# Kernel tuning notes

Measured on AMD Instinct MI355X. Metric: run time of the kernel, lower is better.

## Reference

```python
import jax, jax.numpy as jnp
import numpy as np

DIM = 512
D_IN = 4096
N_OBJ = 2048
N_REL = 32768
STEPS = 2
N_OBJ_CLS = 151
N_REL_CLS = 51
EPS = 1e-5


def _mlp2(x, w1, b1, w2, b2):
    # Linear -> ReLU -> Linear (torch Linear: y = x W^T + b)
    return jnp.maximum(x @ w1.T + b1, 0.0) @ w2.T + b2


def _gate(a, b, w, bias):
    # Sequential(Linear(2*dim, 1), Sigmoid) on cat([a, b], 1)
    return jax.nn.sigmoid(jnp.concatenate([a, b], axis=1) @ w.T + bias)


def _gru_cell(x, h, wih, whh, bih, bhh):
    gi = x @ wih.T + bih  # [N, 3*DIM]
    gh = h @ whh.T + bhh
    ir, iz, inew = jnp.split(gi, 3, axis=1)
    hr, hz, hnew = jnp.split(gh, 3, axis=1)
    r = jax.nn.sigmoid(ir + hr)
    z = jax.nn.sigmoid(iz + hz)
    n = jnp.tanh(inew + r * hnew)
    return (1.0 - z) * n + z * h


def setup_inputs() -> dict:
    key = jax.random.key(0)
    ks = jax.random.split(key, 32)
    rn = lambda k, shape, s=0.02: jax.random.normal(k, shape, dtype=jnp.float32) * s
    z = lambda *shape: jnp.zeros(shape, dtype=jnp.float32)
    return {
        'x_obj': jax.random.normal(ks[0], (N_OBJ, D_IN), dtype=jnp.float32),
        'x_pred': jax.random.normal(ks[1], (N_REL, D_IN), dtype=jnp.float32),
        'rel_inds': jax.random.randint(ks[2], (N_REL, 2), 0, N_OBJ),
        # obj / pred embedding MLPs
        'oe_w1': rn(ks[3], (DIM, D_IN)), 'oe_b1': z(DIM),
        'oe_w2': rn(ks[4], (DIM, DIM)), 'oe_b2': z(DIM),
        'pe_w1': rn(ks[5], (DIM, D_IN)), 'pe_b1': z(DIM),
        'pe_w2': rn(ks[6], (DIM, DIM)), 'pe_b2': z(DIM),
        # gates: Linear(2*dim, 1)
        'g_sn_w': rn(ks[7], (1, 2 * DIM)), 'g_sn_b': z(1),
        'g_on_w': rn(ks[8], (1, 2 * DIM)), 'g_on_b': z(1),
        'g_se_w': rn(ks[9], (1, 2 * DIM)), 'g_se_b': z(1),
        'g_oe_w': rn(ks[10], (1, 2 * DIM)), 'g_oe_b': z(1),
        # GRU cells
        'ngru_wih': rn(ks[11], (3 * DIM, DIM)), 'ngru_whh': rn(ks[12], (3 * DIM, DIM)),
        'ngru_bih': z(3 * DIM), 'ngru_bhh': z(3 * DIM),
        'egru_wih': rn(ks[13], (3 * DIM, DIM)), 'egru_whh': rn(ks[14], (3 * DIM, DIM)),
        'egru_bih': z(3 * DIM), 'egru_bhh': z(3 * DIM),
        # classifier heads
        'op_w': rn(ks[15], (N_OBJ_CLS, DIM)), 'op_b': z(N_OBJ_CLS),
        'pp_w': rn(ks[16], (N_REL_CLS, DIM)), 'pp_b': z(N_REL_CLS),
    }


def reference(x_obj, x_pred, rel_inds,
              oe_w1, oe_b1, oe_w2, oe_b2,
              pe_w1, pe_b1, pe_w2, pe_b2,
              g_sn_w, g_sn_b, g_on_w, g_on_b,
              g_se_w, g_se_b, g_oe_w, g_oe_b,
              ngru_wih, ngru_whh, ngru_bih, ngru_bhh,
              egru_wih, egru_whh, egru_bih, egru_bhh,
              op_w, op_b, pp_w, pp_b):
    n_obj = x_obj.shape[0]
    subj_idx = rel_inds[:, 0]
    obj_idx = rel_inds[:, 1]

    h_obj = _mlp2(x_obj, oe_w1, oe_b1, oe_w2, oe_b2)    # [N_obj, DIM]
    h_edge = _mlp2(x_pred, pe_w1, pe_b1, pe_w2, pe_b2)  # [N_rel, DIM]

    # row sums of the 0/1 subj/obj_pred_map == in-degree counts (constants)
    ones = jnp.ones((rel_inds.shape[0],), dtype=jnp.float32)
    cnt_s = jax.ops.segment_sum(ones, subj_idx, num_segments=n_obj)[:, None]
    cnt_o = jax.ops.segment_sum(ones, obj_idx, num_segments=n_obj)[:, None]

    for _ in range(STEPS):
        sub_vert = h_obj[subj_idx]  # [N_rel, DIM]
        obj_vert = h_obj[obj_idx]

        # node update: gated edge->node messages, mean-aggregated per node
        msg_p2s = _gate(sub_vert, h_edge, g_sn_w, g_sn_b) * h_edge
        msg_p2o = _gate(obj_vert, h_edge, g_on_w, g_on_b) * h_edge
        node_message = (
            jax.ops.segment_sum(msg_p2s, subj_idx, num_segments=n_obj) / (cnt_s + EPS)
            + jax.ops.segment_sum(msg_p2o, obj_idx, num_segments=n_obj) / (cnt_o + EPS)
        ) / 2.0
        new_h_obj = _gru_cell(node_message, h_obj, ngru_wih, ngru_whh, ngru_bih, ngru_bhh)

        # edge update: gated node->edge messages
        msg_s2p = _gate(sub_vert, h_edge, g_se_w, g_se_b) * sub_vert
        msg_o2p = _gate(obj_vert, h_edge, g_oe_w, g_oe_b) * obj_vert
        edge_message = (msg_s2p + msg_o2p) / 2.0
        h_edge = _gru_cell(edge_message, h_edge, egru_wih, egru_whh, egru_bih, egru_bhh)
        h_obj = new_h_obj

    obj_class_logits = h_obj @ op_w.T + op_b    # [N_obj, 151]
    pred_class_logits = h_edge @ pp_w.T + pp_b  # [N_rel, 51]
    obj_class_labels = jnp.argmax(obj_class_logits[:, 1:], axis=1) + 1
    return (h_obj, h_edge, obj_class_logits, pred_class_logits, obj_class_labels, rel_inds)
```

## Files before the change

### kernel.cpp

```cpp
#include <hip/hip_runtime.h>
#include <math.h>

typedef unsigned short u16;
typedef unsigned int u32;
typedef _Float16 f16;
typedef f16 f16x8 __attribute__((ext_vector_type(8)));
typedef float f32x4 __attribute__((ext_vector_type(4)));

#define DIM 512
#define D_IN 4096
#define N_OBJS 2048
#define N_RELS 32768
#define N_OBJ_CLS 151
#define N_REL_CLS 51
#define EPSV 1e-5f

#define OFF_HOBJ  0
#define OFF_HEDGE (N_OBJS*DIM)
#define OFF_OLOG  (OFF_HEDGE + N_RELS*DIM)
#define OFF_PLOG  (OFF_OLOG + N_OBJS*N_OBJ_CLS)
#define OFF_LBL   (OFF_PLOG + N_RELS*N_REL_CLS)
#define OFF_RI    (OFF_LBL + N_OBJS)

__device__ __forceinline__ float sigmoidf_(float x) { return 1.0f / (1.0f + expf(-x)); }
__device__ __forceinline__ u16 f2h_(float f) {
    union { f16 h; u16 u; } c; c.h = (f16)f; return c.u;
}
__device__ __forceinline__ float h2f_(u16 u) {
    union { f16 h; u16 u; } c; c.u = u; return (float)c.h;
}

__device__ __forceinline__ void cvt8h1(const float* f, uint4& h) {
    u32 hh[8];
#pragma unroll
    for (int i = 0; i < 8; i++) hh[i] = f2h_(f[i]);
    h.x = hh[0] | (hh[1] << 16); h.y = hh[2] | (hh[3] << 16);
    h.z = hh[4] | (hh[5] << 16); h.w = hh[6] | (hh[7] << 16);
}
__device__ __forceinline__ void cvt8h2(const float* f, uint4& h, uint4& l) {
    u32 hh[8], ll[8];
#pragma unroll
    for (int i = 0; i < 8; i++) {
        u16 x = f2h_(f[i]);
        hh[i] = x;
        ll[i] = f2h_(f[i] - h2f_(x));
    }
    h.x = hh[0] | (hh[1] << 16); h.y = hh[2] | (hh[3] << 16);
    h.z = hh[4] | (hh[5] << 16); h.w = hh[6] | (hh[7] << 16);
    l.x = ll[0] | (ll[1] << 16); l.y = ll[2] | (ll[3] << 16);
    l.z = ll[4] | (ll[5] << 16); l.w = ll[6] | (ll[7] << 16);
}

__device__ __forceinline__ int swzo(int row, int c) {
    return row * 32 + ((c ^ ((row >> 1) & 3)) << 3);
}

__device__ __forceinline__ int xcdswz(int orig, int nwg) {
    const int q = nwg >> 3;
    return (orig & 7) * q + (orig >> 3);
}

__device__ __forceinline__ void gload16(const void* g, void* l) {
    __builtin_amdgcn_global_load_lds(
        (const __attribute__((address_space(1))) void*)g,
        (__attribute__((address_space(3))) void*)l, 16, 0, 0);
}

__global__ __launch_bounds__(256) void convert_h(const float* __restrict__ src,
    u16* __restrict__ hi, int n4)
{
    const int i = blockIdx.x * 256 + threadIdx.x;
    if (i >= n4) return;
    const float4 v = ((const float4*)src)[i];
    ((ushort4*)hi)[i] = make_ushort4(f2h_(v.x), f2h_(v.y), f2h_(v.z), f2h_(v.w));
}

template<bool RELU, int AT, bool WSPLIT>
__device__ __forceinline__ void gemm_a32_body(
    int id, u16* sAh, u16* sBh, u16* sAl,
    const float* __restrict__ A, const u16* __restrict__ Bhi,
    const float* __restrict__ bias, u16* __restrict__ Chi, u16* __restrict__ Clo,
    int NX, int K)
{
    const int m0 = (id / NX) * 128, n0 = (id % NX) * 128;
    const int N = NX * 128;
    const int t = threadIdx.x;
    const int wid = t >> 6, lane = t & 63;
    const int wm = (wid >> 1) * 64, wn = (wid & 1) * 64;
    const int lr = lane & 15, lk = lane >> 4;

    f32x4 acc[4][4] = {};

    const int sr = t >> 1;
    const int sc = (t & 1) * 2;
    const float* Ap = A + (size_t)(m0 + sr) * K + (t & 1) * 16;

    const int rB = (wid * 2) * 16 + (lane >> 2);
    const int cB = (lane & 3) ^ ((rB >> 1) & 3);
    const u16* Bp0 = Bhi + (size_t)(n0 + rB) * K + cB * 8;
    const u16* Bp1 = Bp0 + (size_t)16 * K;
    u16* Bd0 = &sBh[(wid * 2) * 512];
    u16* Bd1 = Bd0 + 512;

    float fv[16];
    *(float4*)&fv[0]  = *(const float4*)(Ap);
    *(float4*)&fv[4]  = *(const float4*)(Ap + 4);
    *(float4*)&fv[8]  = *(const float4*)(Ap + 8);
    *(float4*)&fv[12] = *(const float4*)(Ap + 12);

    for (int k0 = 0; k0 < K; k0 += 32) {
        uint4 ah0, ah1, al0, al1;
        if (AT == 2) { cvt8h2(fv, ah0, al0); cvt8h2(fv + 8, ah1, al1); }
        else         { cvt8h1(fv, ah0);      cvt8h1(fv + 8, ah1); }

        __syncthreads();
        gload16(Bp0 + k0, Bd0);
        gload16(Bp1 + k0, Bd1);
        *(uint4*)&sAh[swzo(sr, sc)]     = ah0;
        *(uint4*)&sAh[swzo(sr, sc + 1)] = ah1;
        if (AT == 2) {
            *(uint4*)&sAl[swzo(sr, sc)]     = al0;
            *(uint4*)&sAl[swzo(sr, sc + 1)] = al1;
        }
        asm volatile("s_waitcnt vmcnt(0)" ::: "memory");
        __syncthreads();

        const int kn = k0 + 32;
        if (kn < K) {
            *(float4*)&fv[0]  = *(const float4*)(Ap + kn);
            *(float4*)&fv[4]  = *(const float4*)(Ap + kn + 4);
            *(float4*)&fv[8]  = *(const float4*)(Ap + kn + 8);
            *(float4*)&fv[12] = *(const float4*)(Ap + kn + 12);
        }

        f16x8 ah[4], al[4], bh[4];
#pragma unroll
        for (int f = 0; f < 4; f++) {
            const int off = swzo(wm + f * 16 + lr, lk);
            ah[f] = *(const f16x8*)&sAh[off];
            if (AT == 2) al[f] = *(const f16x8*)&sAl[off];
            bh[f] = *(const f16x8*)&sBh[swzo(wn + f * 16 + lr, lk)];
        }
#pragma unroll
        for (int fm = 0; fm < 4; fm++)
#pragma unroll
            for (int fn = 0; fn < 4; fn++) {
                acc[fm][fn] = __builtin_amdgcn_mfma_f32_16x16x32_f16(ah[fm], bh[fn], acc[fm][fn], 0, 0, 0);
                if (AT == 2)
                    acc[fm][fn] = __builtin_amdgcn_mfma_f32_16x16x32_f16(al[fm], bh[fn], acc[fm][fn], 0, 0, 0);
            }
    }
#pragma unroll
    for (int fm = 0; fm < 4; fm++) {
        const int mrow = m0 + wm + fm * 16 + lk * 4;
#pragma unroll
        for (int fn = 0; fn < 4; fn++) {
            const int col = n0 + wn + fn * 16 + lr;
            const float bv = bias[col];
#pragma unroll
            for (int j = 0; j < 4; j++) {
                float v = acc[fm][fn][j] + bv;
                if (RELU) v = fmaxf(v, 0.0f);
                const u16 h = f2h_(v);
                Chi[(size_t)(mrow + j) * N + col] = h;
                if (WSPLIT) Clo[(size_t)(mrow + j) * N + col] = f2h_(v - h2f_(h));
            }
        }
    }
}

__global__ __launch_bounds__(256, 3) void enc1_both(
    const float* __restrict__ xp, const u16* __restrict__ pw,
    const float* __restrict__ pb, u16* __restrict__ tmpe,
    const float* __restrict__ xo, const u16* __restrict__ ow,
    const float* __restrict__ ob, u16* __restrict__ tmpoh, u16* __restrict__ tmpol)
{
    __shared__ u16 smem[3 * 4096];
    const int id = xcdswz(blockIdx.x, gridDim.x);
    if (id < 1024)
        gemm_a32_body<true, 1, false>(id, smem, smem + 4096, nullptr,
                                      xp, pw, pb, tmpe, nullptr, 4, D_IN);
    else
        gemm_a32_body<true, 2, true>(id - 1024, smem, smem + 4096, smem + 8192,
                                     xo, ow, ob, tmpoh, tmpol, 4, D_IN);
}

template<int AT, bool WF32, bool WHI, bool WLO>
__device__ __forceinline__ void gemm_f16_body(
    int id, u16* smem,
    const u16* __restrict__ Ahi, const u16* __restrict__ Alo,
    const u16* __restrict__ Bhi, const float* __restrict__ bias,
    float* __restrict__ C32, u16* __restrict__ Chi, u16* __restrict__ Clo,
    int NX, int N, int ldc, int K)
{
    const int m0 = (id / NX) * 128, n0 = (id % NX) * 128;
    const int t = threadIdx.x;
    const int wid = t >> 6, lane = t & 63;
    const int wm = (wid >> 1) * 64, wn = (wid & 1) * 64;
    const int lr = lane & 15, lk = lane >> 4;

    f32x4 acc[4][4] = {};

    const int rr = (wid * 2) * 16 + (lane >> 2);
    const int cc = (lane & 3) ^ ((rr >> 1) & 3);
    const u16* pA0 = Ahi + (size_t)(m0 + rr) * K + cc * 8;
    const u16* pA1 = pA0 + (size_t)16 * K;
    const u16* pL0 = (AT == 2) ? Alo + (size_t)(m0 + rr) * K + cc * 8 : nullptr;
    const u16* pL1 = (AT == 2) ? pL0 + (size_t)16 * K : nullptr;
    const u16* pB0 = Bhi + (size_t)(n0 + rr) * K + cc * 8;
    const u16* pB1 = pB0 + (size_t)16 * K;
    const int bOff = (wid * 2) * 512;

    for (int k0 = 0; k0 < K; k0 += 64) {
        __syncthreads();
#pragma unroll
        for (int h = 0; h < 2; h++) {
            const int kk = k0 + h * 32;
            u16* sA_ = smem + h * 4096;
            u16* sB_ = smem + 8192 + h * 4096;
            gload16(pA0 + kk, sA_ + bOff);
            gload16(pA1 + kk, sA_ + bOff + 512);
            if (AT == 2) {
                u16* sL_ = smem + 16384 + h * 4096;
                gload16(pL0 + kk, sL_ + bOff);
                gload16(pL1 + kk, sL_ + bOff + 512);
            }
            gload16(pB0 + kk, sB_ + bOff);
            gload16(pB1 + kk, sB_ + bOff + 512);
        }
        asm volatile("s_waitcnt vmcnt(0)" ::: "memory");
        __syncthreads();

#pragma unroll
        for (int h = 0; h < 2; h++) {
            const u16* sA_ = smem + h * 4096;
            const u16* sB_ = smem + 8192 + h * 4096;
            const u16* sL_ = smem + 16384 + h * 4096;
            f16x8 ah[4], al[4], bh[4];
#pragma unroll
            for (int f = 0; f < 4; f++) {
                const int off = swzo(wm + f * 16 + lr, lk);
                ah[f] = *(const f16x8*)&sA_[off];
                if (AT == 2) al[f] = *(const f16x8*)&sL_[off];
                bh[f] = *(const f16x8*)&sB_[swzo(wn + f * 16 + lr, lk)];
            }
#pragma unroll
            for (int fm = 0; fm < 4; fm++)
#pragma unroll
                for (int fn = 0; fn < 4; fn++) {
                    acc[fm][fn] = __builtin_amdgcn_mfma_f32_16x16x32_f16(ah[fm], bh[fn], acc[fm][fn], 0, 0, 0);
                    if (AT == 2)
                        acc[fm][fn] = __builtin_amdgcn_mfma_f32_16x16x32_f16(al[fm], bh[fn], acc[fm][fn], 0, 0, 0);
                }
        }
    }
#pragma unroll
    for (int fm = 0; fm < 4; fm++) {
        const int mrow = m0 + wm + fm * 16 + lk * 4;
#pragma unroll
        for (int fn = 0; fn < 4; fn++) {
            const int col = n0 + wn + fn * 16 + lr;
            const float bv = bias[col];
#pragma unroll
            for (int j = 0; j < 4; j++) {
                const float v = acc[fm][fn][j] + bv;
                if (WF32 && col < N) C32[(size_t)(mrow + j) * ldc + col] = v;
                if (WHI) {
                    const u16 h = f2h_(v);
                    Chi[(size_t)(mrow + j) * (NX * 128) + col] = h;
                    if (WLO)
                        Clo[(size_t)(mrow + j) * (NX * 128) + col] = f2h_(v - h2f_(h));
                }
            }
        }
    }
}

template<int AT, bool WF32, bool WHI, bool WLO>
__global__ __launch_bounds__(256, AT == 1 ? 4 : 3) void gemm_f16(
    const u16* __restrict__ Ahi, const u16* __restrict__ Alo,
    const u16* __restrict__ Bhi, const float* __restrict__ bias,
    float* __restrict__ C32, u16* __restrict__ Chi, u16* __restrict__ Clo,
    int NX, int N, int ldc, int K)
{
    __shared__ u16 smem[AT == 2 ? 6 * 4096 : 4 * 4096];
    const int id = xcdswz(blockIdx.x, gridDim.x);
    gemm_f16_body<AT, WF32, WHI, WLO>(id, smem, Ahi, Alo, Bhi, bias,
                                      C32, Chi, Clo, NX, N, ldc, K);
}

__global__ __launch_bounds__(256, 3) void cls_both(
    const u16* __restrict__ hhe, const u16* __restrict__ pph,
    const float* __restrict__ ppb, float* __restrict__ plog,
    const u16* __restrict__ hhoh, const u16* __restrict__ hhol,
    const u16* __restrict__ oph, const float* __restrict__ opb,
    float* __restrict__ olog)
{
    __shared__ u16 smem[6 * 4096];
    const int id = xcdswz(blockIdx.x, gridDim.x);
    if (id < 256)
        gemm_f16_body<1, true, false, false>(id, smem, hhe, nullptr, pph, ppb,
                                             plog, nullptr, nullptr,
                                             1, N_REL_CLS, N_REL_CLS, DIM);
    else
        gemm_f16_body<2, true, false, false>(id - 256, smem, hhoh, hhol, oph, opb,
                                             olog, nullptr, nullptr,
                                             2, N_OBJ_CLS, N_OBJ_CLS, DIM);
}

template<int AT>
__global__ __launch_bounds__(256, AT == 1 ? 4 : 3) void gru_gemm2(
    const u16* __restrict__ Xh, const u16* __restrict__ Xl,
    const u16* __restrict__ WiH, const float* __restrict__ bi, u16* __restrict__ gi,
    const u16* __restrict__ Hh, const u16* __restrict__ Hl,
    const u16* __restrict__ WhH, const float* __restrict__ bhs, u16* __restrict__ gh_,
    int K)
{
    __shared__ u16 smem[AT == 2 ? 6 * 4096 : 4 * 4096];
    const int id = xcdswz(blockIdx.x, gridDim.x);
    const int part = id % 24;
    const int m0b = id / 24;
    const bool isH = part >= 12;
    const u16* Ahi = isH ? Hh : Xh;
    const u16* Alo = isH ? Hl : Xl;
    const u16* Bhi = isH ? WhH : WiH;
    const float* bias = isH ? bhs : bi;
    u16* C = isH ? gh_ : gi;
    const int nblk = part - (isH ? 12 : 0);
    gemm_f16_body<AT, false, true, false>(m0b * 12 + nblk, smem,
                                          Ahi, Alo, Bhi, bias,
                                          nullptr, C, nullptr, 12, 1536, 1536, K);
}

__device__ __forceinline__ float gcomb(u16 ir, u16 iz, u16 in_, u16 hr, u16 hz,
                                       u16 hn, float h) {
    const float r = sigmoidf_(h2f_(ir) + h2f_(hr));
    const float z = sigmoidf_(h2f_(iz) + h2f_(hz));
    const float n = tanhf(h2f_(in_) + r * h2f_(hn));
    return (1.0f - z) * n + z * h;
}

template<bool WSPLIT, bool WF32>
__global__ __launch_bounds__(256) void gru_combine(
    const u16* __restrict__ gi, const u16* __restrict__ gh,
    u16* __restrict__ hh, u16* __restrict__ hl, float* __restrict__ H32, int R)
{
    const int idx = blockIdx.x * 256 + threadIdx.x;
    if (idx >= R * 128) return;
    const int r = idx >> 7, c4 = (idx & 127) * 4;
    const size_t gb = (size_t)r * 1536 + c4;
    const ushort4 ir4 = *(const ushort4*)&gi[gb];
    const ushort4 iz4 = *(const ushort4*)&gi[gb + 512];
    const ushort4 in4 = *(const ushort4*)&gi[gb + 1024];
    const ushort4 hr4 = *(const ushort4*)&gh[gb];
    const ushort4 hz4 = *(const ushort4*)&gh[gb + 512];
    const ushort4 hn4 = *(const ushort4*)&gh[gb + 1024];
    const size_t hb = (size_t)r * 512 + c4;
    const ushort4 hhi = *(const ushort4*)&hh[hb];
    float h0 = h2f_(hhi.x), h1 = h2f_(hhi.y), h2 = h2f_(hhi.z), h3 = h2f_(hhi.w);
    if (WSPLIT) {
        const ushort4 hlo = *(const ushort4*)&hl[hb];
        h0 += h2f_(hlo.x); h1 += h2f_(hlo.y); h2 += h2f_(hlo.z); h3 += h2f_(hlo.w);
    }
    float4 o;
    o.x = gcomb(ir4.x, iz4.x, in4.x, hr4.x, hz4.x, hn4.x, h0);
    o.y = gcomb(ir4.y, iz4.y, in4.y, hr4.y, hz4.y, hn4.y, h1);
    o.z = gcomb(ir4.z, iz4.z, in4.z, hr4.z, hz4.z, hn4.z, h2);
    o.w = gcomb(ir4.w, iz4.w, in4.w, hr4.w, hz4.w, hn4.w, h3);
    const ushort4 hi4 = make_ushort4(f2h_(o.x), f2h_(o.y), f2h_(o.z), f2h_(o.w));
    *(ushort4*)&hh[hb] = hi4;
    if (WSPLIT) {
        *(ushort4*)&hl[hb] = make_ushort4(
            f2h_(o.x - h2f_(hi4.x)), f2h_(o.y - h2f_(hi4.y)),
            f2h_(o.z - h2f_(hi4.z)), f2h_(o.w - h2f_(hi4.w)));
    }
    if (WF32) *(float4*)&H32[hb] = o;
}

__global__ __launch_bounds__(256) void count_int(const int* __restrict__ rel,
                                                 int* cs, int* co)
{
    const int e = blockIdx.x * 256 + threadIdx.x;
    atomicAdd(&cs[rel[2 * e]], 1);
    atomicAdd(&co[rel[2 * e + 1]], 1);
}

__global__ __launch_bounds__(256) void scan_off(const int* __restrict__ cs,
    const int* __restrict__ co, int* __restrict__ offs, int* __restrict__ offo)
{
    __shared__ int tmp[256];
    for (int arr = 0; arr < 2; arr++) {
        const int* c = arr ? co : cs;
        int* off = arr ? offo : offs;
        const int base = threadIdx.x * 8;
        int loc[8]; int s = 0;
#pragma unroll
        for (int j = 0; j < 8; j++) { loc[j] = c[base + j]; s += loc[j]; }
        tmp[threadIdx.x] = s;
        __syncthreads();
        for (int d = 1; d < 256; d <<= 1) {
            const int v = (threadIdx.x >= d) ? tmp[threadIdx.x - d] : 0;
            __syncthreads();
            tmp[threadIdx.x] += v;
            __syncthreads();
        }
        int p = tmp[threadIdx.x] - s;
#pragma unroll
        for (int j = 0; j < 8; j++) { off[base + j] = p; p += loc[j]; }
        __syncthreads();
    }
}

__global__ __launch_bounds__(256) void fill_csr(const int* __restrict__ rel,
    int* curS, int* curO, const int* __restrict__ offs, const int* __restrict__ offo,
    int* __restrict__ listS, int* __restrict__ listO)
{
    const int e = blockIdx.x * 256 + threadIdx.x;
    const int s = rel[2 * e], o = rel[2 * e + 1];
    const int i = atomicAdd(&curS[s], 1);
    listS[offs[s] + i] = e;
    const int j = atomicAdd(&curO[o], 1);
    listO[offo[o] + j] = e;
}

__global__ __launch_bounds__(256) void gatepass(
    const u16* __restrict__ hho, const u16* __restrict__ hhe,
    const int* __restrict__ rel,
    const float* __restrict__ wsn, const float* __restrict__ bsn,
    const float* __restrict__ won, const float* __restrict__ bon,
    const float* __restrict__ wse, const float* __restrict__ bse,
    const float* __restrict__ woe, const float* __restrict__ boe,
    const int* __restrict__ cs, const int* __restrict__ co,
    u16* __restrict__ emh, float* __restrict__ af, float* __restrict__ ag)
{
    const int e = blockIdx.x * 4 + (threadIdx.x >> 6);
    const int lane = threadIdx.x & 63;
    const int s = rel[2 * e], o = rel[2 * e + 1];
    const int c = lane * 8;

    const uint4 hsu = *(const uint4*)&hho[(size_t)s * DIM + c];
    const uint4 hou = *(const uint4*)&hho[(size_t)o * DIM + c];
    const uint4 heu = *(const uint4*)&hhe[(size_t)e * DIM + c];
    float hs[8], ho[8], he[8];
    hs[0] = h2f_((u16)hsu.x); hs[1] = h2f_((u16)(hsu.x >> 16));
    hs[2] = h2f_((u16)hsu.y); hs[3] = h2f_((u16)(hsu.y >> 16));
    hs[4] = h2f_((u16)hsu.z); hs[5] = h2f_((u16)(hsu.z >> 16));
    hs[6] = h2f_((u16)hsu.w); hs[7] = h2f_((u16)(hsu.w >> 16));
    ho[0] = h2f_((u16)hou.x); ho[1] = h2f_((u16)(hou.x >> 16));
    ho[2] = h2f_((u16)hou.y); ho[3] = h2f_((u16)(hou.y >> 16));
    ho[4] = h2f_((u16)hou.z); ho[5] = h2f_((u16)(hou.z >> 16));
    ho[6] = h2f_((u16)hou.w); ho[7] = h2f_((u16)(hou.w >> 16));
    he[0] = h2f_((u16)heu.x); he[1] = h2f_((u16)(heu.x >> 16));
    he[2] = h2f_((u16)heu.y); he[3] = h2f_((u16)(heu.y >> 16));
    he[4] = h2f_((u16)heu.z); he[5] = h2f_((u16)(heu.z >> 16));
    he[6] = h2f_((u16)heu.w); he[7] = h2f_((u16)(heu.w >> 16));

    float p0 = 0.f, p1 = 0.f, p2 = 0.f, p3 = 0.f;
#pragma unroll
    for (int q = 0; q < 2; q++) {
        const float4 w0v = *(const float4*)&wsn[c + q * 4];
        const float4 w0e = *(const float4*)&wsn[DIM + c + q * 4];
        const float4 w1v = *(const float4*)&won[c + q * 4];
        const float4 w1e = *(const float4*)&won[DIM + c + q * 4];
        const float4 w2v = *(const float4*)&wse[c + q * 4];
        const float4 w2e = *(const float4*)&wse[DIM + c + q * 4];
        const float4 w3v = *(const float4*)&woe[c + q * 4];
        const float4 w3e = *(const float4*)&woe[DIM + c + q * 4];
        const float* s4 = &hs[q * 4];
        const float* o4 = &ho[q * 4];
        const float* e4 = &he[q * 4];
        p0 += s4[0]*w0v.x + s4[1]*w0v.y + s4[2]*w0v.z + s4[3]*w0v.w
            + e4[0]*w0e.x + e4[1]*w0e.y + e4[2]*w0e.z + e4[3]*w0e.w;
        p1 += o4[0]*w1v.x + o4[1]*w1v.y + o4[2]*w1v.z + o4[3]*w1v.w
            + e4[0]*w1e.x + e4[1]*w1e.y + e4[2]*w1e.z + e4[3]*w1e.w;
        p2 += s4[0]*w2v.x + s4[1]*w2v.y + s4[2]*w2v.z + s4[3]*w2v.w
            + e4[0]*w2e.x + e4[1]*w2e.y + e4[2]*w2e.z + e4[3]*w2e.w;
        p3 += o4[0]*w3v.x + o4[1]*w3v.y + o4[2]*w3v.z + o4[3]*w3v.w
            + e4[0]*w3e.x + e4[1]*w3e.y + e4[2]*w3e.z + e4[3]*w3e.w;
    }
#pragma unroll
    for (int off = 32; off; off >>= 1) {
        p0 += __shfl_xor(p0, off);
        p1 += __shfl_xor(p1, off);
        p2 += __shfl_xor(p2, off);
        p3 += __shfl_xor(p3, off);
    }
    const float gsn = sigmoidf_(p0 + bsn[0]);
    const float gon = sigmoidf_(p1 + bon[0]);
    const float gse = sigmoidf_(p2 + bse[0]);
    const float goe = sigmoidf_(p3 + boe[0]);

    if (lane == 0) {
        af[e] = 0.5f * gsn / ((float)cs[s] + EPSV);
        ag[e] = 0.5f * gon / ((float)co[o] + EPSV);
    }
    u16 em8[8];
#pragma unroll
    for (int j = 0; j < 8; j++)
        em8[j] = f2h_(0.5f * (gse * hs[j] + goe * ho[j]));
    *(uint4*)&emh[(size_t)e * DIM + c] = *(const uint4*)em8;
}

__global__ __launch_bounds__(256) void gather_nm(
    const u16* __restrict__ hhe,
    const int* __restrict__ listS, const int* __restrict__ listO,
    const int* __restrict__ offs, const int* __restrict__ offo,
    const int* __restrict__ cs, const int* __restrict__ co,
    const float* __restrict__ af, const float* __restrict__ ag,
    u16* __restrict__ nmh, u16* __restrict__ nml)
{
    const int v = blockIdx.x * 4 + (threadIdx.x >> 6);
    const int lane = threadIdx.x & 63;
    const int c = lane * 8;

    float acc[8] = {};
#pragma unroll
    for (int side = 0; side < 2; side++) {
        const int* list = side ? listO : listS;
        const int b = side ? offo[v] : offs[v];
        const int n = side ? co[v] : cs[v];
        const float* coef = side ? ag : af;
        for (int i = 0; i < n; i++) {
            const int e = list[b + i];
            const float a = coef[e];
            const uint4 x = *(const uint4*)&hhe[(size_t)e * DIM + c];
            acc[0] += a * h2f_((u16)x.x); acc[1] += a * h2f_((u16)(x.x >> 16));
            acc[2] += a * h2f_((u16)x.y); acc[3] += a * h2f_((u16)(x.y >> 16));
            acc[4] += a * h2f_((u16)x.z); acc[5] += a * h2f_((u16)(x.z >> 16));
            acc[6] += a * h2f_((u16)x.w); acc[7] += a * h2f_((u16)(x.w >> 16));
        }
    }
    u16 hi8[8], lo8[8];
#pragma unroll
    for (int j = 0; j < 8; j++) {
        hi8[j] = f2h_(acc[j]);
        lo8[j] = f2h_(acc[j] - h2f_(hi8[j]));
    }
    *(uint4*)&nmh[(size_t)v * DIM + c] = *(const uint4*)hi8;
    *(uint4*)&nml[(size_t)v * DIM + c] = *(const uint4*)lo8;
}

__global__ __launch_bounds__(256) void argmax_kernel(const float* __restrict__ logits,
                                                     float* __restrict__ out)
{
    const int row = blockIdx.x * 4 + (threadIdx.x >> 6);
    const int lane = threadIdx.x & 63;
    float bv = -1e30f; int bi = 1;
    for (int j = 1 + lane; j < N_OBJ_CLS; j += 64) {
        const float v = logits[(size_t)row * N_OBJ_CLS + j];
        if (v > bv) { bv = v; bi = j; }
    }
#pragma unroll
    for (int off = 32; off; off >>= 1) {
        const float ov = __shfl_xor(bv, off);
        const int oi = __shfl_xor(bi, off);
        if (ov > bv || (ov == bv && oi < bi)) { bv = ov; bi = oi; }
    }
    if (lane == 0) out[row] = (float)bi;
}

__global__ __launch_bounds__(256) void relinds_kernel(const int* __restrict__ rel,
                                                      float* __restrict__ out)
{
    const int i = blockIdx.x * 256 + threadIdx.x;
    out[i] = (float)rel[i];
}

extern "C" void kernel_launch(void* const* d_in, const int* in_sizes, int n_in,
                              void* d_out, int out_size, void* d_ws, size_t ws_size,
                              hipStream_t stream)
{
    const float* x_obj = (const float*)d_in[0];
    const float* x_pred = (const float*)d_in[1];
    const int* rel = (const int*)d_in[2];
    const float* oe_w1 = (const float*)d_in[3];
    const float* oe_b1 = (const float*)d_in[4];
    const float* oe_w2 = (const float*)d_in[5];
    const float* oe_b2 = (const float*)d_in[6];
    const float* pe_w1 = (const float*)d_in[7];
    const float* pe_b1 = (const float*)d_in[8];
    const float* pe_w2 = (const float*)d_in[9];
    const float* pe_b2 = (const float*)d_in[10];
    const float* g_sn_w = (const float*)d_in[11];
    const float* g_sn_b = (const float*)d_in[12];
    const float* g_on_w = (const float*)d_in[13];
    const float* g_on_b = (const float*)d_in[14];
    const float* g_se_w = (const float*)d_in[15];
    const float* g_se_b = (const float*)d_in[16];
    const float* g_oe_w = (const float*)d_in[17];
    const float* g_oe_b = (const float*)d_in[18];
    const float* ngru_wih = (const float*)d_in[19];
    const float* ngru_whh = (const float*)d_in[20];
    const float* ngru_bih = (const float*)d_in[21];
    const float* ngru_bhh = (const float*)d_in[22];
    const float* egru_wih = (const float*)d_in[23];
    const float* egru_whh = (const float*)d_in[24];
    const float* egru_bih = (const float*)d_in[25];
    const float* egru_bhh = (const float*)d_in[26];
    const float* op_w = (const float*)d_in[27];
    const float* op_b = (const float*)d_in[28];
    const float* pp_w = (const float*)d_in[29];
    const float* pp_b = (const float*)d_in[30];

    float* out = (float*)d_out;

    float* h_obj = out + OFF_HOBJ;
    float* h_edge = out + OFF_HEDGE;

    char* wsp = (char*)d_ws;
    float* af = (float*)wsp; wsp += N_RELS * 4;
    float* ag = (float*)wsp; wsp += N_RELS * 4;
    int* cs = (int*)wsp;   wsp += N_OBJS * 4;
    int* co = (int*)wsp;   wsp += N_OBJS * 4;
    int* offs = (int*)wsp; wsp += N_OBJS * 4;
    int* offo = (int*)wsp; wsp += N_OBJS * 4;
    int* curS = (int*)wsp; wsp += N_OBJS * 4;
    int* curO = (int*)wsp; wsp += N_OBJS * 4;
    int* listS = (int*)wsp; wsp += N_RELS * 4;
    int* listO = (int*)wsp; wsp += N_RELS * 4;

    u16* wp = (u16*)wsp;
    const int s_big = DIM * D_IN, s_sq = DIM * DIM, s_gru = 3 * DIM * DIM;
    u16 *oe1h = wp; wp += s_big;
    u16 *pe1h = wp; wp += s_big;
    u16 *oe2h = wp; wp += s_sq;
    u16 *pe2h = wp; wp += s_sq;
    u16 *nih_h = wp; wp += s_gru;
    u16 *nhh_h = wp; wp += s_gru;
    u16 *eih_h = wp; wp += s_gru;
    u16 *ehh_h = wp; wp += s_gru;
    u16 *oph = wp; wp += 256 * DIM;
    u16 *pph = wp; wp += 128 * DIM;
    u16 *tmpo_h = wp; wp += (size_t)N_OBJS * DIM;
    u16 *tmpo_l = wp; wp += (size_t)N_OBJS * DIM;
    u16 *tmpe_h = wp; wp += (size_t)N_RELS * DIM;
    u16 *hhoh = wp; wp += (size_t)N_OBJS * DIM;
    u16 *hhol = wp; wp += (size_t)N_OBJS * DIM;
    u16 *hhe  = wp; wp += (size_t)N_RELS * DIM;
    u16 *emh  = wp; wp += (size_t)N_RELS * DIM;
    u16 *nmh  = wp; wp += (size_t)N_OBJS * DIM;
    u16 *nml  = wp; wp += (size_t)N_OBJS * DIM;

    const size_t used = (size_t)((char*)wp - (char*)d_ws);
    int R = 8192;
    if (used + (size_t)16384 * 6144 <= ws_size) R = 16384;
    u16* gi = wp;
    u16* gh = gi + (size_t)R * 1536;

    auto cvtw = [&](const float* s, u16* h, int n) {
        convert_h<<<(n / 4 + 255) / 256, 256, 0, stream>>>(s, h, n / 4);
    };
    cvtw(oe_w1, oe1h, s_big);
    cvtw(pe_w1, pe1h, s_big);
    cvtw(oe_w2, oe2h, s_sq);
    cvtw(pe_w2, pe2h, s_sq);
    cvtw(ngru_wih, nih_h, s_gru);
    cvtw(ngru_whh, nhh_h, s_gru);
    cvtw(egru_wih, eih_h, s_gru);
    cvtw(egru_whh, ehh_h, s_gru);
    cvtw(op_w, oph, N_OBJ_CLS * DIM);
    cvtw(pp_w, pph, N_REL_CLS * DIM);

    hipMemsetAsync(cs, 0, 2 * N_OBJS * sizeof(int), stream);
    hipMemsetAsync(curS, 0, 2 * N_OBJS * sizeof(int), stream);
    count_int<<<N_RELS / 256, 256, 0, stream>>>(rel, cs, co);
    scan_off<<<1, 256, 0, stream>>>(cs, co, offs, offo);
    fill_csr<<<N_RELS / 256, 256, 0, stream>>>(rel, curS, curO, offs, offo, listS, listO);

    enc1_both<<<1088, 256, 0, stream>>>(
        x_pred, pe1h, pe_b1, tmpe_h,
        x_obj, oe1h, oe_b1, tmpo_h, tmpo_l);
    gemm_f16<1, false, true, false><<<4 * (N_RELS / 128), 256, 0, stream>>>(
        tmpe_h, nullptr, pe2h, pe_b2, nullptr, hhe, nullptr, 4, DIM, DIM, DIM);
    gemm_f16<2, false, true, true><<<4 * (N_OBJS / 128), 256, 0, stream>>>(
        tmpo_h, tmpo_l, oe2h, oe_b2, nullptr, hhoh, hhol, 4, DIM, DIM, DIM);

    for (int step = 0; step < 2; step++) {
        gatepass<<<N_RELS / 4, 256, 0, stream>>>(
            hhoh, hhe, rel,
            g_sn_w, g_sn_b, g_on_w, g_on_b, g_se_w, g_se_b, g_oe_w, g_oe_b,
            cs, co, emh, af, ag);
        gather_nm<<<N_OBJS / 4, 256, 0, stream>>>(
            hhe, listS, listO, offs, offo, cs, co, af, ag, nmh, nml);

        gru_gemm2<2><<<24 * (N_OBJS / 128), 256, 0, stream>>>(
            nmh, nml, nih_h, ngru_bih, gi, hhoh, hhol, nhh_h, ngru_bhh, gh, DIM);
        if (step == 0)
            gru_combine<true, false><<<(N_OBJS * 128 + 255) / 256, 256, 0, stream>>>(
                gi, gh, hhoh, hhol, nullptr, N_OBJS);
        else
            gru_combine<true, true><<<(N_OBJS * 128 + 255) / 256, 256, 0, stream>>>(
                gi, gh, hhoh, hhol, h_obj, N_OBJS);

        for (int r0 = 0; r0 < N_RELS; r0 += R) {
            const int Rc = (N_RELS - r0 < R) ? (N_RELS - r0) : R;
            gru_gemm2<1><<<24 * (Rc / 128), 256, 0, stream>>>(
                emh + (size_t)r0 * DIM, nullptr, eih_h, egru_bih, gi,
                hhe + (size_t)r0 * DIM, nullptr, ehh_h, egru_bhh, gh, DIM);
            if (step == 0)
                gru_combine<false, false><<<(Rc * 128 + 255) / 256, 256, 0, stream>>>(
                    gi, gh, hhe + (size_t)r0 * DIM, nullptr, nullptr, Rc);
            else
                gru_combine<false, true><<<(Rc * 128 + 255) / 256, 256, 0, stream>>>(
                    gi, gh, hhe + (size_t)r0 * DIM, nullptr, h_edge + (size_t)r0 * DIM, Rc);
        }
    }

    cls_both<<<288, 256, 0, stream>>>(
        hhe, pph, pp_b, out + OFF_PLOG,
        hhoh, hhol, oph, op_b, out + OFF_OLOG);

    argmax_kernel<<<N_OBJS / 4, 256, 0, stream>>>(out + OFF_OLOG, out + OFF_LBL);
    relinds_kernel<<<(2 * N_RELS) / 256, 256, 0, stream>>>(rel, out + OFF_RI);
}
```

Baseline: 1.002 ms.

## Fuse GRU r/z gate GEMMs over concatenated [x,h] with packed weights

Concatenates the input and hidden rows along K and packs the r/z slices of W_ih and W_hh into one 1024x1024 weight, so the r and z pre-activations come out of a single K=1024 GEMM with summed biases. The n-gate input and hidden parts stay as separate K=512 GEMMs. All outputs go to one 2048-wide buffer, and the combine kernel reads four slices instead of six. This cuts GEMM output writes and combine reads from 3072 to 2048 columns per row with the same FLOPs, at the cost of a new GEMM body and extra weight packing kernels.

```diff
diff --git a/kernel.cpp b/kernel.cpp
--- a/kernel.cpp
+++ b/kernel.cpp
@@ -14,6 +14,7 @@
 #define N_OBJ_CLS 151
 #define N_REL_CLS 51
 #define EPSV 1e-5f
+#define GOUT 2048
 
 #define OFF_HOBJ  0
 #define OFF_HEDGE (N_OBJS*DIM)
@@ -73,6 +74,23 @@
     if (i >= n4) return;
     const float4 v = ((const float4*)src)[i];
     ((ushort4*)hi)[i] = make_ushort4(f2h_(v.x), f2h_(v.y), f2h_(v.z), f2h_(v.w));
+}
+
+__global__ __launch_bounds__(256) void pack_rz(const u16* __restrict__ ih,
+    const u16* __restrict__ hh, u16* __restrict__ wrz)
+{
+    const int idx = blockIdx.x * 256 + threadIdx.x;
+    const int n = idx >> 7, kk = (idx & 127) * 8;
+    const uint4 v = (kk < 512) ? *(const uint4*)&ih[(size_t)n * 512 + kk]
+                               : *(const uint4*)&hh[(size_t)n * 512 + kk - 512];
+    *(uint4*)&wrz[(size_t)n * 1024 + kk] = v;
+}
+
+__global__ __launch_bounds__(256) void pack_brz(const float* __restrict__ bih,
+    const float* __restrict__ bhh, float* __restrict__ brz)
+{
+    const int j = blockIdx.x * 256 + threadIdx.x;
+    brz[j] = bih[j] + bhh[j];
 }
 
 template<bool RELU, int AT, bool WSPLIT>
@@ -309,52 +327,134 @@
 }
 
 template<int AT>
-__global__ __launch_bounds__(256, AT == 1 ? 4 : 3) void gru_gemm2(
+__device__ __forceinline__ void gru_body(
+    int m0b, int nblk, u16* smem,
     const u16* __restrict__ Xh, const u16* __restrict__ Xl,
-    const u16* __restrict__ WiH, const float* __restrict__ bi, u16* __restrict__ gi,
     const u16* __restrict__ Hh, const u16* __restrict__ Hl,
-    const u16* __restrict__ WhH, const float* __restrict__ bhs, u16* __restrict__ gh_,
-    int K)
+    const u16* __restrict__ B, const float* __restrict__ bias,
+    u16* __restrict__ C, int K)
+{
+    const int m0 = m0b * 128, n0 = nblk * 128;
+    const int t = threadIdx.x;
+    const int wid = t >> 6, lane = t & 63;
+    const int wm = (wid >> 1) * 64, wn = (wid & 1) * 64;
+    const int lr = lane & 15, lk = lane >> 4;
+
+    f32x4 acc[4][4] = {};
+
+    const int rr = (wid * 2) * 16 + (lane >> 2);
+    const int cc = (lane & 3) ^ ((rr >> 1) & 3);
+    const size_t arow = (size_t)(m0 + rr) * DIM + cc * 8;
+    const u16* pX0 = Xh + arow; const u16* pX1 = pX0 + 16 * DIM;
+    const u16* pXl0 = (AT == 2) ? Xl + arow : nullptr;
+    const u16* pXl1 = (AT == 2) ? pXl0 + 16 * DIM : nullptr;
+    const u16* pH0 = Hh + arow; const u16* pH1 = pH0 + 16 * DIM;
+    const u16* pHl0 = (AT == 2) ? Hl + arow : nullptr;
+    const u16* pHl1 = (AT == 2) ? pHl0 + 16 * DIM : nullptr;
+    const u16* pB0 = B + (size_t)(n0 + rr) * K + cc * 8;
+    const u16* pB1 = pB0 + (size_t)16 * K;
+    const int bOff = (wid * 2) * 512;
+
+    for (int k0 = 0; k0 < K; k0 += 64) {
+        __syncthreads();
+#pragma unroll
+        for (int h = 0; h < 2; h++) {
+            const int kk = k0 + h * 32;
+            const bool inX = kk < 512;
+            const int ka = inX ? kk : kk - 512;
+            u16* sA_ = smem + h * 4096;
+            u16* sB_ = smem + 8192 + h * 4096;
+            gload16((inX ? pX0 : pH0) + ka, sA_ + bOff);
+            gload16((inX ? pX1 : pH1) + ka, sA_ + bOff + 512);
+            if (AT == 2) {
+                u16* sL_ = smem + 16384 + h * 4096;
+                gload16((inX ? pXl0 : pHl0) + ka, sL_ + bOff);
+                gload16((inX ? pXl1 : pHl1) + ka, sL_ + bOff + 512);
+            }
+            gload16(pB0 + kk, sB_ + bOff);
+            gload16(pB1 + kk, sB_ + bOff + 512);
+        }
+        asm volatile("s_waitcnt vmcnt(0)" ::: "memory");
+        __syncthreads();
+
+#pragma unroll
+        for (int h = 0; h < 2; h++) {
+            const u16* sA_ = smem + h * 4096;
+            const u16* sB_ = smem + 8192 + h * 4096;
+            const u16* sL_ = smem + 16384 + h * 4096;
+            f16x8 ah[4], al[4], bh[4];
+#pragma unroll
+            for (int f = 0; f < 4; f++) {
+                const int off = swzo(wm + f * 16 + lr, lk);
+                ah[f] = *(const f16x8*)&sA_[off];
+                if (AT == 2) al[f] = *(const f16x8*)&sL_[off];
+                bh[f] = *(const f16x8*)&sB_[swzo(wn + f * 16 + lr, lk)];
+            }
+#pragma unroll
+            for (int fm = 0; fm < 4; fm++)
+#pragma unroll
+                for (int fn = 0; fn < 4; fn++) {
+                    acc[fm][fn] = __builtin_amdgcn_mfma_f32_16x16x32_f16(ah[fm], bh[fn], acc[fm][fn], 0, 0, 0);
+                    if (AT == 2)
+                        acc[fm][fn] = __builtin_amdgcn_mfma_f32_16x16x32_f16(al[fm], bh[fn], acc[fm][fn], 0, 0, 0);
+                }
+        }
+    }
+#pragma unroll
+    for (int fm = 0; fm < 4; fm++) {
+        const int mrow = m0 + wm + fm * 16 + lk * 4;
+#pragma unroll
+        for (int fn = 0; fn < 4; fn++) {
+            const int col = n0 + wn + fn * 16 + lr;
+            const float bv = bias[col];
+#pragma unroll
+            for (int j = 0; j < 4; j++)
+                C[(size_t)(mrow + j) * GOUT + col] = f2h_(acc[fm][fn][j] + bv);
+        }
+    }
+}
+
+template<int AT>
+__global__ __launch_bounds__(256, AT == 1 ? 4 : 3) void gru_gemm3(
+    const u16* __restrict__ Xh, const u16* __restrict__ Xl,
+    const u16* __restrict__ Hh, const u16* __restrict__ Hl,
+    const u16* __restrict__ Wrz, const float* __restrict__ brz,
+    const u16* __restrict__ Wni, const float* __restrict__ bni,
+    const u16* __restrict__ Wnh, const float* __restrict__ bnh,
+    u16* __restrict__ C)
 {
     __shared__ u16 smem[AT == 2 ? 6 * 4096 : 4 * 4096];
     const int id = xcdswz(blockIdx.x, gridDim.x);
-    const int part = id % 24;
-    const int m0b = id / 24;
-    const bool isH = part >= 12;
-    const u16* Ahi = isH ? Hh : Xh;
-    const u16* Alo = isH ? Hl : Xl;
-    const u16* Bhi = isH ? WhH : WiH;
-    const float* bias = isH ? bhs : bi;
-    u16* C = isH ? gh_ : gi;
-    const int nblk = part - (isH ? 12 : 0);
-    gemm_f16_body<AT, false, true, false>(m0b * 12 + nblk, smem,
-                                          Ahi, Alo, Bhi, bias,
-                                          nullptr, C, nullptr, 12, 1536, 1536, K);
-}
-
-__device__ __forceinline__ float gcomb(u16 ir, u16 iz, u16 in_, u16 hr, u16 hz,
-                                       u16 hn, float h) {
-    const float r = sigmoidf_(h2f_(ir) + h2f_(hr));
-    const float z = sigmoidf_(h2f_(iz) + h2f_(hz));
+    const int part = id % 16;
+    const int m0b = id / 16;
+    if (part < 8)
+        gru_body<AT>(m0b, part, smem, Xh, Xl, Hh, Hl, Wrz, brz, C, 1024);
+    else if (part < 12)
+        gru_body<AT>(m0b, part - 8, smem, Xh, Xl, Xh, Xl, Wni, bni, C + 1024, 512);
+    else
+        gru_body<AT>(m0b, part - 12, smem, Hh, Hl, Hh, Hl, Wnh, bnh, C + 1536, 512);
+}
+
+__device__ __forceinline__ float gcomb2(u16 rzr, u16 rzz, u16 in_, u16 hn, float h) {
+    const float r = sigmoidf_(h2f_(rzr));
+    const float z = sigmoidf_(h2f_(rzz));
     const float n = tanhf(h2f_(in_) + r * h2f_(hn));
     return (1.0f - z) * n + z * h;
 }
 
 template<bool WSPLIT, bool WF32>
-__global__ __launch_bounds__(256) void gru_combine(
-    const u16* __restrict__ gi, const u16* __restrict__ gh,
-    u16* __restrict__ hh, u16* __restrict__ hl, float* __restrict__ H32, int R)
+__global__ __launch_bounds__(256) void gru_combine2(
+    const u16* __restrict__ g, u16* __restrict__ hh, u16* __restrict__ hl,
+    float* __restrict__ H32, int R)
 {
     const int idx = blockIdx.x * 256 + threadIdx.x;
     if (idx >= R * 128) return;
     const int r = idx >> 7, c4 = (idx & 127) * 4;
-    const size_t gb = (size_t)r * 1536 + c4;
-    const ushort4 ir4 = *(const ushort4*)&gi[gb];
-    const ushort4 iz4 = *(const ushort4*)&gi[gb + 512];
-    const ushort4 in4 = *(const ushort4*)&gi[gb + 1024];
-    const ushort4 hr4 = *(const ushort4*)&gh[gb];
-    const ushort4 hz4 = *(const ushort4*)&gh[gb + 512];
-    const ushort4 hn4 = *(const ushort4*)&gh[gb + 1024];
+    const size_t gb = (size_t)r * GOUT + c4;
+    const ushort4 r4 = *(const ushort4*)&g[gb];
+    const ushort4 z4 = *(const ushort4*)&g[gb + 512];
+    const ushort4 in4 = *(const ushort4*)&g[gb + 1024];
+    const ushort4 hn4 = *(const ushort4*)&g[gb + 1536];
     const size_t hb = (size_t)r * 512 + c4;
     const ushort4 hhi = *(const ushort4*)&hh[hb];
     float h0 = h2f_(hhi.x), h1 = h2f_(hhi.y), h2 = h2f_(hhi.z), h3 = h2f_(hhi.w);
@@ -363,10 +463,10 @@
         h0 += h2f_(hlo.x); h1 += h2f_(hlo.y); h2 += h2f_(hlo.z); h3 += h2f_(hlo.w);
     }
     float4 o;
-    o.x = gcomb(ir4.x, iz4.x, in4.x, hr4.x, hz4.x, hn4.x, h0);
-    o.y = gcomb(ir4.y, iz4.y, in4.y, hr4.y, hz4.y, hn4.y, h1);
-    o.z = gcomb(ir4.z, iz4.z, in4.z, hr4.z, hz4.z, hn4.z, h2);
-    o.w = gcomb(ir4.w, iz4.w, in4.w, hr4.w, hz4.w, hn4.w, h3);
+    o.x = gcomb2(r4.x, z4.x, in4.x, hn4.x, h0);
+    o.y = gcomb2(r4.y, z4.y, in4.y, hn4.y, h1);
+    o.z = gcomb2(r4.z, z4.z, in4.z, hn4.z, h2);
+    o.w = gcomb2(r4.w, z4.w, in4.w, hn4.w, h3);
     const ushort4 hi4 = make_ushort4(f2h_(o.x), f2h_(o.y), f2h_(o.z), f2h_(o.w));
     *(ushort4*)&hh[hb] = hi4;
     if (WSPLIT) {
@@ -610,6 +710,8 @@
     char* wsp = (char*)d_ws;
     float* af = (float*)wsp; wsp += N_RELS * 4;
     float* ag = (float*)wsp; wsp += N_RELS * 4;
+    float* brz_n = (float*)wsp; wsp += 1024 * 4;
+    float* brz_e = (float*)wsp; wsp += 1024 * 4;
     int* cs = (int*)wsp;   wsp += N_OBJS * 4;
     int* co = (int*)wsp;   wsp += N_OBJS * 4;
     int* offs = (int*)wsp; wsp += N_OBJS * 4;
@@ -631,6 +733,8 @@
     u16 *ehh_h = wp; wp += s_gru;
     u16 *oph = wp; wp += 256 * DIM;
     u16 *pph = wp; wp += 128 * DIM;
+    u16 *wrz_n = wp; wp += 1024 * 1024;
+    u16 *wrz_e = wp; wp += 1024 * 1024;
     u16 *tmpo_h = wp; wp += (size_t)N_OBJS * DIM;
     u16 *tmpo_l = wp; wp += (size_t)N_OBJS * DIM;
     u16 *tmpe_h = wp; wp += (size_t)N_RELS * DIM;
@@ -643,9 +747,8 @@
 
     const size_t used = (size_t)((char*)wp - (char*)d_ws);
     int R = 8192;
-    if (used + (size_t)16384 * 6144 <= ws_size) R = 16384;
-    u16* gi = wp;
-    u16* gh = gi + (size_t)R * 1536;
+    if (used + (size_t)16384 * (GOUT * 2) <= ws_size) R = 16384;
+    u16* gcat = wp;
 
     auto cvtw = [&](const float* s, u16* h, int n) {
         convert_h<<<(n / 4 + 255) / 256, 256, 0, stream>>>(s, h, n / 4);
@@ -660,6 +763,10 @@
     cvtw(egru_whh, ehh_h, s_gru);
     cvtw(op_w, oph, N_OBJ_CLS * DIM);
     cvtw(pp_w, pph, N_REL_CLS * DIM);
+    pack_rz<<<512, 256, 0, stream>>>(nih_h, nhh_h, wrz_n);
+    pack_rz<<<512, 256, 0, stream>>>(eih_h, ehh_h, wrz_e);
+    pack_brz<<<4, 256, 0, stream>>>(ngru_bih, ngru_bhh, brz_n);
+    pack_brz<<<4, 256, 0, stream>>>(egru_bih, egru_bhh, brz_e);
 
     hipMemsetAsync(cs, 0, 2 * N_OBJS * sizeof(int), stream);
     hipMemsetAsync(curS, 0, 2 * N_OBJS * sizeof(int), stream);
@@ -683,26 +790,30 @@
         gather_nm<<<N_OBJS / 4, 256, 0, stream>>>(
             hhe, listS, listO, offs, offo, cs, co, af, ag, nmh, nml);
 
-        gru_gemm2<2><<<24 * (N_OBJS / 128), 256, 0, stream>>>(
-            nmh, nml, nih_h, ngru_bih, gi, hhoh, hhol, nhh_h, ngru_bhh, gh, DIM);
+        gru_gemm3<2><<<16 * (N_OBJS / 128), 256, 0, stream>>>(
+            nmh, nml, hhoh, hhol, wrz_n, brz_n,
+            nih_h + 1024 * DIM, ngru_bih + 1024,
+            nhh_h + 1024 * DIM, ngru_bhh + 1024, gcat);
         if (step == 0)
-            gru_combine<true, false><<<(N_OBJS * 128 + 255) / 256, 256, 0, stream>>>(
-                gi, gh, hhoh, hhol, nullptr, N_OBJS);
+            gru_combine2<true, false><<<(N_OBJS * 128 + 255) / 256, 256, 0, stream>>>(
+                gcat, hhoh, hhol, nullptr, N_OBJS);
         else
-            gru_combine<true, true><<<(N_OBJS * 128 + 255) / 256, 256, 0, stream>>>(
-                gi, gh, hhoh, hhol, h_obj, N_OBJS);
+            gru_combine2<true, true><<<(N_OBJS * 128 + 255) / 256, 256, 0, stream>>>(
+                gcat, hhoh, hhol, h_obj, N_OBJS);
 
         for (int r0 = 0; r0 < N_RELS; r0 += R) {
             const int Rc = (N_RELS - r0 < R) ? (N_RELS - r0) : R;
-            gru_gemm2<1><<<24 * (Rc / 128), 256, 0, stream>>>(
-                emh + (size_t)r0 * DIM, nullptr, eih_h, egru_bih, gi,
-                hhe + (size_t)r0 * DIM, nullptr, ehh_h, egru_bhh, gh, DIM);
+            gru_gemm3<1><<<16 * (Rc / 128), 256, 0, stream>>>(
+                emh + (size_t)r0 * DIM, nullptr, hhe + (size_t)r0 * DIM, nullptr,
+                wrz_e, brz_e,
+                eih_h + 1024 * DIM, egru_bih + 1024,
+                ehh_h + 1024 * DIM, egru_bhh + 1024, gcat);
             if (step == 0)
-                gru_combine<false, false><<<(Rc * 128 + 255) / 256, 256, 0, stream>>>(
-                    gi, gh, hhe + (size_t)r0 * DIM, nullptr, nullptr, Rc);
+                gru_combine2<false, false><<<(Rc * 128 + 255) / 256, 256, 0, stream>>>(
+                    gcat, hhe + (size_t)r0 * DIM, nullptr, nullptr, Rc);
             else
-                gru_combine<false, true><<<(Rc * 128 + 255) / 256, 256, 0, stream>>>(
-                    gi, gh, hhe + (size_t)r0 * DIM, nullptr, h_edge + (size_t)r0 * DIM, Rc);
+                gru_combine2<false, true><<<(Rc * 128 + 255) / 256, 256, 0, stream>>>(
+                    gcat, hhe + (size_t)r0 * DIM, nullptr, h_edge + (size_t)r0 * DIM, Rc);
         }
     }
 
```

After: 1.007 ms. Within noise of the previous version (+0.5%).
